# Kernel tuning notes

Hardware: AMD Instinct MI355X
Metric: run time of the kernel (lower is better)

Reference implementation:

```python
import jax, jax.numpy as jnp
import numpy as np
from jax import lax

WINDOW_SIZE = 11
SIGMA = 1.5
C1 = 0.01 ** 2
C2 = 0.03 ** 2


def _gaussian_window(size, sigma):
    coords = np.arange(size, dtype=np.float32) - size // 2
    g = np.exp(-coords ** 2 / (2.0 * sigma ** 2)).astype(np.float32)
    g = g / g.sum()
    w = np.outer(g, g)  # [size, size]
    return jnp.asarray(w)


def _depthwise_conv(x, window2d):
    # x: [B, C, H, W]; window2d: [k, k]
    C = x.shape[1]
    k = window2d.shape[0]
    kernel = jnp.broadcast_to(window2d[None, None], (C, 1, k, k)).astype(x.dtype)
    pad = k // 2
    return lax.conv_general_dilated(
        x, kernel,
        window_strides=(1, 1),
        padding=[(pad, pad), (pad, pad)],
        dimension_numbers=('NCHW', 'OIHW', 'NCHW'),
        feature_group_count=C,
    )


def setup_inputs() -> dict:
    key = jax.random.key(0)
    k1, k2 = jax.random.split(key)
    shape = (32, 3, 512, 512)
    pred = jax.random.uniform(k1, shape, dtype=jnp.float32)
    target = jax.random.uniform(k2, shape, dtype=jnp.float32)
    return {"pred": pred, "target": target}


def reference(pred, target):
    window = _gaussian_window(WINDOW_SIZE, SIGMA)
    mu1 = _depthwise_conv(pred, window)
    mu2 = _depthwise_conv(target, window)
    mu1_sq = mu1 * mu1
    mu2_sq = mu2 * mu2
    mu1_mu2 = mu1 * mu2
    sigma1_sq = _depthwise_conv(pred * pred, window) - mu1_sq
    sigma2_sq = _depthwise_conv(target * target, window) - mu2_sq
    sigma12 = _depthwise_conv(pred * target, window) - mu1_mu2
    ssim_map = ((2.0 * mu1_mu2 + C1) * (2.0 * sigma12 + C2)) / (
        (mu1_sq + mu2_sq + C1) * (sigma1_sq + sigma2_sq + C2))
    return 1.0 - ssim_map.mean()
```

## Files before the change

kernel.cpp:

```cpp
#include <hip/hip_runtime.h>


typedef float f32x2 __attribute__((ext_vector_type(2)));
typedef unsigned int u32;

#define IH 512
#define IW 512
#define TH 4
#define TW 256
#define PW 266
#define RRN 14
#define LPW 268
#define HTILES 128
#define NTILE 24576
#define CPX 3072
#define NPIX 25165824.0f
#define NTHR 320

constexpr float GW[11] = {
    0.00102838f, 0.00759877f, 0.03600078f, 0.10936070f, 0.21300554f,
    0.26601173f,
    0.21300554f, 0.10936070f, 0.03600078f, 0.00759877f, 0.00102838f
};
constexpr float C1f = 0.0001f;
constexpr float C2f = 0.0009f;

__global__ __launch_bounds__(1024) void ssim_reduce(
    const float* __restrict__ ws, float* __restrict__ out)
{
    __shared__ float wsum[16];
    const int tid = threadIdx.x;
    const float4* w4 = reinterpret_cast<const float4*>(ws);
    float s = 0.0f;
    #pragma unroll
    for (int i = 0; i < 6; ++i) {
        const float4 v = w4[tid + i * 1024];
        s += (v.x + v.y) + (v.z + v.w);
    }
    #pragma unroll
    for (int off = 32; off > 0; off >>= 1) s += __shfl_down(s, off, 64);
    if ((tid & 63) == 0) wsum[tid >> 6] = s;
    __syncthreads();
    if (tid == 0) {
        float t = 0.f;
        #pragma unroll
        for (int i = 0; i < 16; ++i) t += wsum[i];
        out[0] = 1.0f - t * (1.0f / NPIX);
    }
}

__global__ __launch_bounds__(NTHR, 2) void ssim_main(
    const float* __restrict__ pred,
    const float* __restrict__ targ,
    float* __restrict__ ws)
{
    __shared__ __align__(16) f32x2 lds01[TH][LPW];
    __shared__ __align__(16) f32x2 lds23[TH][LPW];
    __shared__ float wsum[5];

    const int tid = threadIdx.x;

    const int b  = blockIdx.x;
    const int tl = (b & 7) * CPX + (b >> 3);
    const int ht = tl & (HTILES - 1);
    const int wt = (tl >> 7) & 1;
    const int bc = tl >> 8;

    const int rbase = ht * TH - 5;
    const float* __restrict__ P = pred + (size_t)bc * (IH * IW);
    const float* __restrict__ T = targ + (size_t)bc * (IH * IW);

    if (tid < PW) {
        const int w = wt * TW - 5 + tid;
        const float wm = ((unsigned)w < (unsigned)IW) ? 1.0f : 0.0f;
        const int wc = w < 0 ? 0 : (w > IW - 1 ? IW - 1 : w);

        float rm[RRN];
        u32 voff[RRN];
        #pragma unroll
        for (int rr = 0; rr < RRN; ++rr) {
            const int h = rbase + rr;
            rm[rr] = ((unsigned)h < (unsigned)IH) ? 1.0f : 0.0f;
            const int hc = h < 0 ? 0 : (h > IH - 1 ? IH - 1 : h);
            voff[rr] = (u32)((hc * IW + wc) * 4);
        }

        float pv[RRN], tv[RRN];
        #pragma unroll
        for (int rr = 0; rr < RRN; ++rr)
            asm volatile("global_load_dword %0, %1, %2"
                         : "=v"(pv[rr]) : "v"(voff[rr]), "s"(P));
        #pragma unroll
        for (int rr = 0; rr < RRN; ++rr)
            asm volatile("global_load_dword %0, %1, %2"
                         : "=v"(tv[rr]) : "v"(voff[rr]), "s"(T));
        asm volatile("s_waitcnt vmcnt(0)" ::: "memory");
        __builtin_amdgcn_sched_barrier(0);

        f32x2 a01[TH], a23[TH];
        #pragma unroll
        for (int ro = 0; ro < TH; ++ro) {
            a01[ro].x = 0.f; a01[ro].y = 0.f;
            a23[ro].x = 0.f; a23[ro].y = 0.f;
        }

        #pragma unroll
        for (int rr = 0; rr < RRN; ++rr) {
            f32x2 s01; s01.x = pv[rr]; s01.y = tv[rr];
            const f32x2 rmv = {rm[rr], rm[rr]};
            s01 = s01 * rmv;
            f32x2 s23;
            s23.x = fmaf(s01.x, s01.x, s01.y * s01.y);
            s23.y = s01.x * s01.y;
            #pragma unroll
            for (int ro = 0; ro < TH; ++ro) {
                const int k = rr - ro;
                if (k >= 0 && k < 11) {
                    const f32x2 g = {GW[k], GW[k]};
                    a01[ro] = __builtin_elementwise_fma(g, s01, a01[ro]);
                    a23[ro] = __builtin_elementwise_fma(g, s23, a23[ro]);
                }
            }
        }
        const f32x2 wmv = {wm, wm};
        #pragma unroll
        for (int ro = 0; ro < TH; ++ro) {
            lds01[ro][tid] = a01[ro] * wmv;
            lds23[ro][tid] = a23[ro] * wmv;
        }
    }
    __syncthreads();

    float lsum = 0.0f;
    if (tid < 256) {
        const int r  = tid >> 6;
        const int c0 = (tid & 63) << 2;

        float4 u4[7], v4[7];
        const float4* b01 = reinterpret_cast<const float4*>(&lds01[r][c0]);
        const float4* b23 = reinterpret_cast<const float4*>(&lds23[r][c0]);
        #pragma unroll
        for (int q = 0; q < 7; ++q) { u4[q] = b01[q]; v4[q] = b23[q]; }
        const f32x2* x01 = reinterpret_cast<const f32x2*>(u4);
        const f32x2* x23 = reinterpret_cast<const f32x2*>(v4);

        #pragma unroll
        for (int j = 0; j < 4; ++j) {
            f32x2 acc01; acc01.x = 0.f; acc01.y = 0.f;
            f32x2 acc23; acc23.x = 0.f; acc23.y = 0.f;
            #pragma unroll
            for (int k = 0; k < 11; ++k) {
                const f32x2 g = {GW[k], GW[k]};
                acc01 = __builtin_elementwise_fma(g, x01[j + k], acc01);
                acc23 = __builtin_elementwise_fma(g, x23[j + k], acc23);
            }
            const float m1  = acc01.x;
            const float m2  = acc01.y;
            const float sPP = acc23.x;
            const float e12 = acc23.y;
            const float m1m2 = m1 * m2;
            const float msq  = fmaf(m1, m1, m2 * m2);
            const float num = fmaf(2.0f, m1m2, C1f) * fmaf(2.0f, (e12 - m1m2), C2f);
            const float den = (msq + C1f) * ((sPP - msq) + C2f);
            lsum = fmaf(num, __builtin_amdgcn_rcpf(den), lsum);
        }
    }

    #pragma unroll
    for (int off = 32; off > 0; off >>= 1) lsum += __shfl_down(lsum, off, 64);
    const int lane = tid & 63;
    const int wv   = tid >> 6;
    if (lane == 0) wsum[wv] = lsum;
    __syncthreads();
    if (tid == 0) {
        const float bs = wsum[0] + wsum[1] + wsum[2] + wsum[3] + wsum[4];
        ws[b] = bs;
    }
}

extern "C" void kernel_launch(void* const* d_in, const int* in_sizes, int n_in,
                              void* d_out, int out_size, void* d_ws, size_t ws_size,
                              hipStream_t stream) {
    const float* pred = (const float*)d_in[0];
    const float* targ = (const float*)d_in[1];
    float* out = (float*)d_out;
    float* wsf = (float*)d_ws;

    hipLaunchKernelGGL(ssim_main, dim3(NTILE), dim3(NTHR), 0, stream,
                       pred, targ, wsf);
    hipLaunchKernelGGL(ssim_reduce, dim3(1), dim3(1024), 0, stream, wsf, out);
}
```

Baseline: 89.03 us.

## Stream row slabs per block with sliding register window and prefetch

Each block now walks a vertical slab of 16 row-tiles (64 output rows) instead of a single 4-row tile. It keeps a 14-row register window that shifts by 4 rows per step and prefetches the next 4 rows during compute. This cuts the 14/4 vertical halo re-reads of global memory and the per-tile block launch overhead, so the grid drops from 24576 to 1536 blocks. In exchange there are two barriers per step, fewer blocks for latency hiding, a serial loop dependency, and the row-mask multiply only on border slabs.

```diff
diff --git a/kernel.cpp b/kernel.cpp
--- a/kernel.cpp
+++ b/kernel.cpp
@@ -2,18 +2,17 @@
 
 
 typedef float f32x2 __attribute__((ext_vector_type(2)));
-typedef unsigned int u32;
 
 #define IH 512
 #define IW 512
 #define TH 4
 #define TW 256
 #define PW 266
-#define RRN 14
 #define LPW 268
-#define HTILES 128
-#define NTILE 24576
-#define CPX 3072
+#define KT 16
+#define NSLAB 8
+#define NBLK 1536
+#define CPX 192
 #define NPIX 25165824.0f
 #define NTHR 320
 
@@ -25,28 +24,25 @@
 constexpr float C1f = 0.0001f;
 constexpr float C2f = 0.0009f;
 
-__global__ __launch_bounds__(1024) void ssim_reduce(
+__global__ __launch_bounds__(256) void ssim_reduce(
     const float* __restrict__ ws, float* __restrict__ out)
 {
-    __shared__ float wsum[16];
+    __shared__ float wsum[4];
     const int tid = threadIdx.x;
-    const float4* w4 = reinterpret_cast<const float4*>(ws);
     float s = 0.0f;
     #pragma unroll
-    for (int i = 0; i < 6; ++i) {
-        const float4 v = w4[tid + i * 1024];
-        s += (v.x + v.y) + (v.z + v.w);
-    }
+    for (int i = 0; i < 6; ++i) s += ws[tid + i * 256];
     #pragma unroll
     for (int off = 32; off > 0; off >>= 1) s += __shfl_down(s, off, 64);
     if ((tid & 63) == 0) wsum[tid >> 6] = s;
     __syncthreads();
     if (tid == 0) {
-        float t = 0.f;
-        #pragma unroll
-        for (int i = 0; i < 16; ++i) t += wsum[i];
-        out[0] = 1.0f - t * (1.0f / NPIX);
-    }
+        out[0] = 1.0f - (wsum[0] + wsum[1] + wsum[2] + wsum[3]) * (1.0f / NPIX);
+    }
+}
+
+__device__ __forceinline__ int hclamp(int h) {
+    return h < 0 ? 0 : (h > IH - 1 ? IH - 1 : h);
 }
 
 __global__ __launch_bounds__(NTHR, 2) void ssim_main(
@@ -62,107 +58,125 @@
 
     const int b  = blockIdx.x;
     const int tl = (b & 7) * CPX + (b >> 3);
-    const int ht = tl & (HTILES - 1);
-    const int wt = (tl >> 7) & 1;
-    const int bc = tl >> 8;
-
-    const int rbase = ht * TH - 5;
+    const int slab = tl & (NSLAB - 1);
+    const int wt   = (tl >> 3) & 1;
+    const int bc   = tl >> 4;
+    const int j0   = slab * KT;
+
     const float* __restrict__ P = pred + (size_t)bc * (IH * IW);
     const float* __restrict__ T = targ + (size_t)bc * (IH * IW);
 
-    if (tid < PW) {
-        const int w = wt * TW - 5 + tid;
-        const float wm = ((unsigned)w < (unsigned)IW) ? 1.0f : 0.0f;
-        const int wc = w < 0 ? 0 : (w > IW - 1 ? IW - 1 : w);
-
-        float rm[RRN];
-        u32 voff[RRN];
-        #pragma unroll
-        for (int rr = 0; rr < RRN; ++rr) {
-            const int h = rbase + rr;
-            rm[rr] = ((unsigned)h < (unsigned)IH) ? 1.0f : 0.0f;
-            const int hc = h < 0 ? 0 : (h > IH - 1 ? IH - 1 : h);
-            voff[rr] = (u32)((hc * IW + wc) * 4);
-        }
-
-        float pv[RRN], tv[RRN];
-        #pragma unroll
-        for (int rr = 0; rr < RRN; ++rr)
-            asm volatile("global_load_dword %0, %1, %2"
-                         : "=v"(pv[rr]) : "v"(voff[rr]), "s"(P));
-        #pragma unroll
-        for (int rr = 0; rr < RRN; ++rr)
-            asm volatile("global_load_dword %0, %1, %2"
-                         : "=v"(tv[rr]) : "v"(voff[rr]), "s"(T));
-        asm volatile("s_waitcnt vmcnt(0)" ::: "memory");
+    const int w = wt * TW - 5 + tid;
+    const float wm = ((unsigned)w < (unsigned)IW) ? 1.0f : 0.0f;
+    const int wc = w < 0 ? 0 : (w > IW - 1 ? IW - 1 : w);
+    const bool active = tid < PW;
+    const bool border = (slab == 0) || (slab == NSLAB - 1);
+
+    float pv[14], tv[14];
+    float nlp[4], nlt[4];
+    #pragma unroll
+    for (int rr = 0; rr < 14; ++rr) {
+        const int hc = hclamp(4 * j0 - 5 + rr);
+        pv[rr] = P[(size_t)hc * IW + wc];
+        tv[rr] = T[(size_t)hc * IW + wc];
+    }
+    __builtin_amdgcn_sched_barrier(0);
+
+    float lsum = 0.0f;
+    const f32x2 wmv = {wm, wm};
+
+    for (int jj = 0; jj < KT; ++jj) {
+        const int j = j0 + jj;
+
+        if (jj < KT - 1) {
+            #pragma unroll
+            for (int i = 0; i < 4; ++i) {
+                const int hc = hclamp(4 * j + 9 + i);
+                nlp[i] = P[(size_t)hc * IW + wc];
+                nlt[i] = T[(size_t)hc * IW + wc];
+            }
+        }
         __builtin_amdgcn_sched_barrier(0);
 
-        f32x2 a01[TH], a23[TH];
-        #pragma unroll
-        for (int ro = 0; ro < TH; ++ro) {
-            a01[ro].x = 0.f; a01[ro].y = 0.f;
-            a23[ro].x = 0.f; a23[ro].y = 0.f;
-        }
-
-        #pragma unroll
-        for (int rr = 0; rr < RRN; ++rr) {
-            f32x2 s01; s01.x = pv[rr]; s01.y = tv[rr];
-            const f32x2 rmv = {rm[rr], rm[rr]};
-            s01 = s01 * rmv;
-            f32x2 s23;
-            s23.x = fmaf(s01.x, s01.x, s01.y * s01.y);
-            s23.y = s01.x * s01.y;
+        {
+            f32x2 a01[TH], a23[TH];
             #pragma unroll
             for (int ro = 0; ro < TH; ++ro) {
-                const int k = rr - ro;
-                if (k >= 0 && k < 11) {
+                a01[ro].x = 0.f; a01[ro].y = 0.f;
+                a23[ro].x = 0.f; a23[ro].y = 0.f;
+            }
+            #pragma unroll
+            for (int rr = 0; rr < 14; ++rr) {
+                float p = pv[rr], t = tv[rr];
+                if (border) {
+                    const int row = 4 * j - 5 + rr;
+                    const float rmk = ((unsigned)row < (unsigned)IH) ? 1.0f : 0.0f;
+                    p *= rmk; t *= rmk;
+                }
+                f32x2 s01; s01.x = p; s01.y = t;
+                f32x2 s23;
+                s23.x = fmaf(p, p, t * t);
+                s23.y = p * t;
+                #pragma unroll
+                for (int ro = 0; ro < TH; ++ro) {
+                    const int k = rr - ro;
+                    if (k >= 0 && k < 11) {
+                        const f32x2 g = {GW[k], GW[k]};
+                        a01[ro] = __builtin_elementwise_fma(g, s01, a01[ro]);
+                        a23[ro] = __builtin_elementwise_fma(g, s23, a23[ro]);
+                    }
+                }
+            }
+            if (active) {
+                #pragma unroll
+                for (int ro = 0; ro < TH; ++ro) {
+                    lds01[ro][tid] = a01[ro] * wmv;
+                    lds23[ro][tid] = a23[ro] * wmv;
+                }
+            }
+        }
+        __syncthreads();
+
+        if (tid < 256) {
+            const int r  = tid >> 6;
+            const int c0 = (tid & 63) << 2;
+
+            float4 u4[7], v4[7];
+            const float4* b01 = reinterpret_cast<const float4*>(&lds01[r][c0]);
+            const float4* b23 = reinterpret_cast<const float4*>(&lds23[r][c0]);
+            #pragma unroll
+            for (int q = 0; q < 7; ++q) { u4[q] = b01[q]; v4[q] = b23[q]; }
+            const f32x2* x01 = reinterpret_cast<const f32x2*>(u4);
+            const f32x2* x23 = reinterpret_cast<const f32x2*>(v4);
+
+            #pragma unroll
+            for (int jo = 0; jo < 4; ++jo) {
+                f32x2 acc01; acc01.x = 0.f; acc01.y = 0.f;
+                f32x2 acc23; acc23.x = 0.f; acc23.y = 0.f;
+                #pragma unroll
+                for (int k = 0; k < 11; ++k) {
                     const f32x2 g = {GW[k], GW[k]};
-                    a01[ro] = __builtin_elementwise_fma(g, s01, a01[ro]);
-                    a23[ro] = __builtin_elementwise_fma(g, s23, a23[ro]);
-                }
-            }
-        }
-        const f32x2 wmv = {wm, wm};
-        #pragma unroll
-        for (int ro = 0; ro < TH; ++ro) {
-            lds01[ro][tid] = a01[ro] * wmv;
-            lds23[ro][tid] = a23[ro] * wmv;
-        }
-    }
-    __syncthreads();
-
-    float lsum = 0.0f;
-    if (tid < 256) {
-        const int r  = tid >> 6;
-        const int c0 = (tid & 63) << 2;
-
-        float4 u4[7], v4[7];
-        const float4* b01 = reinterpret_cast<const float4*>(&lds01[r][c0]);
-        const float4* b23 = reinterpret_cast<const float4*>(&lds23[r][c0]);
-        #pragma unroll
-        for (int q = 0; q < 7; ++q) { u4[q] = b01[q]; v4[q] = b23[q]; }
-        const f32x2* x01 = reinterpret_cast<const f32x2*>(u4);
-        const f32x2* x23 = reinterpret_cast<const f32x2*>(v4);
-
-        #pragma unroll
-        for (int j = 0; j < 4; ++j) {
-            f32x2 acc01; acc01.x = 0.f; acc01.y = 0.f;
-            f32x2 acc23; acc23.x = 0.f; acc23.y = 0.f;
-            #pragma unroll
-            for (int k = 0; k < 11; ++k) {
-                const f32x2 g = {GW[k], GW[k]};
-                acc01 = __builtin_elementwise_fma(g, x01[j + k], acc01);
-                acc23 = __builtin_elementwise_fma(g, x23[j + k], acc23);
-            }
-            const float m1  = acc01.x;
-            const float m2  = acc01.y;
-            const float sPP = acc23.x;
-            const float e12 = acc23.y;
-            const float m1m2 = m1 * m2;
-            const float msq  = fmaf(m1, m1, m2 * m2);
-            const float num = fmaf(2.0f, m1m2, C1f) * fmaf(2.0f, (e12 - m1m2), C2f);
-            const float den = (msq + C1f) * ((sPP - msq) + C2f);
-            lsum = fmaf(num, __builtin_amdgcn_rcpf(den), lsum);
+                    acc01 = __builtin_elementwise_fma(g, x01[jo + k], acc01);
+                    acc23 = __builtin_elementwise_fma(g, x23[jo + k], acc23);
+                }
+                const float m1  = acc01.x;
+                const float m2  = acc01.y;
+                const float sPP = acc23.x;
+                const float e12 = acc23.y;
+                const float m1m2 = m1 * m2;
+                const float msq  = fmaf(m1, m1, m2 * m2);
+                const float num = fmaf(2.0f, m1m2, C1f) * fmaf(2.0f, (e12 - m1m2), C2f);
+                const float den = (msq + C1f) * ((sPP - msq) + C2f);
+                lsum = fmaf(num, __builtin_amdgcn_rcpf(den), lsum);
+            }
+        }
+        __syncthreads();
+
+        if (jj < KT - 1) {
+            #pragma unroll
+            for (int i = 0; i < 10; ++i) { pv[i] = pv[i + 4]; tv[i] = tv[i + 4]; }
+            #pragma unroll
+            for (int i = 0; i < 4; ++i)  { pv[10 + i] = nlp[i]; tv[10 + i] = nlt[i]; }
         }
     }
 
@@ -173,8 +187,7 @@
     if (lane == 0) wsum[wv] = lsum;
     __syncthreads();
     if (tid == 0) {
-        const float bs = wsum[0] + wsum[1] + wsum[2] + wsum[3] + wsum[4];
-        ws[b] = bs;
+        ws[b] = wsum[0] + wsum[1] + wsum[2] + wsum[3] + wsum[4];
     }
 }
 
@@ -186,7 +199,7 @@
     float* out = (float*)d_out;
     float* wsf = (float*)d_ws;
 
-    hipLaunchKernelGGL(ssim_main, dim3(NTILE), dim3(NTHR), 0, stream,
+    hipLaunchKernelGGL(ssim_main, dim3(NBLK), dim3(NTHR), 0, stream,
                        pred, targ, wsf);
-    hipLaunchKernelGGL(ssim_reduce, dim3(1), dim3(1024), 0, stream, wsf, out);
-}
+    hipLaunchKernelGGL(ssim_reduce, dim3(1), dim3(256), 0, stream, wsf, out);
+}
```

Result: slower. 129.0 us (+44.8%).

## Cover full image width per block with two columns per thread

Applied to the files above, without the earlier changes.

Each block now processes a full 512-wide row strip instead of a 256-wide half, and each thread loads two adjacent columns as float2. This removes the halo columns that were loaded twice at the split and halves the block count. Width masking is replaced by zero-filled edge pairs, and row masking now runs only on the border tiles. The horizontal pass computes 8 outputs per thread from wider LDS reads. Register use per thread grows, while launch bounds now ask for 4 blocks per CU.

```diff
diff --git a/kernel.cpp b/kernel.cpp
--- a/kernel.cpp
+++ b/kernel.cpp
@@ -2,18 +2,17 @@
 
 
 typedef float f32x2 __attribute__((ext_vector_type(2)));
-typedef unsigned int u32;
 
 #define IH 512
 #define IW 512
 #define TH 4
-#define TW 256
-#define PW 266
-#define RRN 14
-#define LPW 268
+#define NPAIR 262
+#define PSTART 3
+#define PEND 258
+#define LPW 524
 #define HTILES 128
-#define NTILE 24576
-#define CPX 3072
+#define NBLK 12288
+#define CPX 1536
 #define NPIX 25165824.0f
 #define NTHR 320
 
@@ -33,7 +32,7 @@
     const float4* w4 = reinterpret_cast<const float4*>(ws);
     float s = 0.0f;
     #pragma unroll
-    for (int i = 0; i < 6; ++i) {
+    for (int i = 0; i < 3; ++i) {
         const float4 v = w4[tid + i * 1024];
         s += (v.x + v.y) + (v.z + v.w);
     }
@@ -49,7 +48,7 @@
     }
 }
 
-__global__ __launch_bounds__(NTHR, 2) void ssim_main(
+__global__ __launch_bounds__(NTHR, 4) void ssim_main(
     const float* __restrict__ pred,
     const float* __restrict__ targ,
     float* __restrict__ ws)
@@ -63,70 +62,74 @@
     const int b  = blockIdx.x;
     const int tl = (b & 7) * CPX + (b >> 3);
     const int ht = tl & (HTILES - 1);
-    const int wt = (tl >> 7) & 1;
-    const int bc = tl >> 8;
+    const int bc = tl >> 7;
 
     const int rbase = ht * TH - 5;
+    const bool border = (ht == 0) || (ht == HTILES - 1);
     const float* __restrict__ P = pred + (size_t)bc * (IH * IW);
     const float* __restrict__ T = targ + (size_t)bc * (IH * IW);
 
-    if (tid < PW) {
-        const int w = wt * TW - 5 + tid;
-        const float wm = ((unsigned)w < (unsigned)IW) ? 1.0f : 0.0f;
-        const int wc = w < 0 ? 0 : (w > IW - 1 ? IW - 1 : w);
+    if (tid < NPAIR) {
+        const bool hot = (tid >= PSTART) && (tid <= PEND);
+        if (hot) {
+            const int wA = 2 * tid - 6;
+            f32x2 pv[14], tv[14];
+            #pragma unroll
+            for (int rr = 0; rr < 14; ++rr) {
+                const int h = rbase + rr;
+                const int hc = h < 0 ? 0 : (h > IH - 1 ? IH - 1 : h);
+                pv[rr] = *reinterpret_cast<const f32x2*>(P + (size_t)hc * IW + wA);
+                tv[rr] = *reinterpret_cast<const f32x2*>(T + (size_t)hc * IW + wA);
+            }
+            __builtin_amdgcn_sched_barrier(0);
 
-        float rm[RRN];
-        u32 voff[RRN];
-        #pragma unroll
-        for (int rr = 0; rr < RRN; ++rr) {
-            const int h = rbase + rr;
-            rm[rr] = ((unsigned)h < (unsigned)IH) ? 1.0f : 0.0f;
-            const int hc = h < 0 ? 0 : (h > IH - 1 ? IH - 1 : h);
-            voff[rr] = (u32)((hc * IW + wc) * 4);
-        }
-
-        float pv[RRN], tv[RRN];
-        #pragma unroll
-        for (int rr = 0; rr < RRN; ++rr)
-            asm volatile("global_load_dword %0, %1, %2"
-                         : "=v"(pv[rr]) : "v"(voff[rr]), "s"(P));
-        #pragma unroll
-        for (int rr = 0; rr < RRN; ++rr)
-            asm volatile("global_load_dword %0, %1, %2"
-                         : "=v"(tv[rr]) : "v"(voff[rr]), "s"(T));
-        asm volatile("s_waitcnt vmcnt(0)" ::: "memory");
-        __builtin_amdgcn_sched_barrier(0);
-
-        f32x2 a01[TH], a23[TH];
-        #pragma unroll
-        for (int ro = 0; ro < TH; ++ro) {
-            a01[ro].x = 0.f; a01[ro].y = 0.f;
-            a23[ro].x = 0.f; a23[ro].y = 0.f;
-        }
-
-        #pragma unroll
-        for (int rr = 0; rr < RRN; ++rr) {
-            f32x2 s01; s01.x = pv[rr]; s01.y = tv[rr];
-            const f32x2 rmv = {rm[rr], rm[rr]};
-            s01 = s01 * rmv;
-            f32x2 s23;
-            s23.x = fmaf(s01.x, s01.x, s01.y * s01.y);
-            s23.y = s01.x * s01.y;
+            f32x2 aA01[TH], aB01[TH], aA23[TH], aB23[TH];
             #pragma unroll
             for (int ro = 0; ro < TH; ++ro) {
-                const int k = rr - ro;
-                if (k >= 0 && k < 11) {
-                    const f32x2 g = {GW[k], GW[k]};
-                    a01[ro] = __builtin_elementwise_fma(g, s01, a01[ro]);
-                    a23[ro] = __builtin_elementwise_fma(g, s23, a23[ro]);
+                aA01[ro] = (f32x2){0.f, 0.f}; aB01[ro] = (f32x2){0.f, 0.f};
+                aA23[ro] = (f32x2){0.f, 0.f}; aB23[ro] = (f32x2){0.f, 0.f};
+            }
+            #pragma unroll
+            for (int rr = 0; rr < 14; ++rr) {
+                float pA = pv[rr].x, pB = pv[rr].y;
+                float tA = tv[rr].x, tB = tv[rr].y;
+                if (border) {
+                    const float rmk =
+                        ((unsigned)(rbase + rr) < (unsigned)IH) ? 1.0f : 0.0f;
+                    pA *= rmk; pB *= rmk; tA *= rmk; tB *= rmk;
+                }
+                const f32x2 sA01 = {pA, tA};
+                const f32x2 sB01 = {pB, tB};
+                const f32x2 sA23 = {fmaf(pA, pA, tA * tA), pA * tA};
+                const f32x2 sB23 = {fmaf(pB, pB, tB * tB), pB * tB};
+                #pragma unroll
+                for (int ro = 0; ro < TH; ++ro) {
+                    const int k = rr - ro;
+                    if (k >= 0 && k < 11) {
+                        const f32x2 g = {GW[k], GW[k]};
+                        aA01[ro] = __builtin_elementwise_fma(g, sA01, aA01[ro]);
+                        aB01[ro] = __builtin_elementwise_fma(g, sB01, aB01[ro]);
+                        aA23[ro] = __builtin_elementwise_fma(g, sA23, aA23[ro]);
+                        aB23[ro] = __builtin_elementwise_fma(g, sB23, aB23[ro]);
+                    }
                 }
             }
-        }
-        const f32x2 wmv = {wm, wm};
-        #pragma unroll
-        for (int ro = 0; ro < TH; ++ro) {
-            lds01[ro][tid] = a01[ro] * wmv;
-            lds23[ro][tid] = a23[ro] * wmv;
+            #pragma unroll
+            for (int ro = 0; ro < TH; ++ro) {
+                float4 u; u.x = aA01[ro].x; u.y = aA01[ro].y;
+                          u.z = aB01[ro].x; u.w = aB01[ro].y;
+                float4 v; v.x = aA23[ro].x; v.y = aA23[ro].y;
+                          v.z = aB23[ro].x; v.w = aB23[ro].y;
+                *reinterpret_cast<float4*>(&lds01[ro][2 * tid]) = u;
+                *reinterpret_cast<float4*>(&lds23[ro][2 * tid]) = v;
+            }
+        } else {
+            const float4 z = {0.f, 0.f, 0.f, 0.f};
+            #pragma unroll
+            for (int ro = 0; ro < TH; ++ro) {
+                *reinterpret_cast<float4*>(&lds01[ro][2 * tid]) = z;
+                *reinterpret_cast<float4*>(&lds23[ro][2 * tid]) = z;
+            }
         }
     }
     __syncthreads();
@@ -134,25 +137,25 @@
     float lsum = 0.0f;
     if (tid < 256) {
         const int r  = tid >> 6;
-        const int c0 = (tid & 63) << 2;
+        const int c0 = (tid & 63) << 3;
 
-        float4 u4[7], v4[7];
+        float4 u4[10], v4[10];
         const float4* b01 = reinterpret_cast<const float4*>(&lds01[r][c0]);
         const float4* b23 = reinterpret_cast<const float4*>(&lds23[r][c0]);
         #pragma unroll
-        for (int q = 0; q < 7; ++q) { u4[q] = b01[q]; v4[q] = b23[q]; }
+        for (int q = 0; q < 10; ++q) { u4[q] = b01[q]; v4[q] = b23[q]; }
         const f32x2* x01 = reinterpret_cast<const f32x2*>(u4);
         const f32x2* x23 = reinterpret_cast<const f32x2*>(v4);
 
         #pragma unroll
-        for (int j = 0; j < 4; ++j) {
-            f32x2 acc01; acc01.x = 0.f; acc01.y = 0.f;
-            f32x2 acc23; acc23.x = 0.f; acc23.y = 0.f;
+        for (int j = 0; j < 8; ++j) {
+            f32x2 acc01 = {0.f, 0.f};
+            f32x2 acc23 = {0.f, 0.f};
             #pragma unroll
             for (int k = 0; k < 11; ++k) {
                 const f32x2 g = {GW[k], GW[k]};
-                acc01 = __builtin_elementwise_fma(g, x01[j + k], acc01);
-                acc23 = __builtin_elementwise_fma(g, x23[j + k], acc23);
+                acc01 = __builtin_elementwise_fma(g, x01[j + k + 1], acc01);
+                acc23 = __builtin_elementwise_fma(g, x23[j + k + 1], acc23);
             }
             const float m1  = acc01.x;
             const float m2  = acc01.y;
@@ -173,8 +176,7 @@
     if (lane == 0) wsum[wv] = lsum;
     __syncthreads();
     if (tid == 0) {
-        const float bs = wsum[0] + wsum[1] + wsum[2] + wsum[3] + wsum[4];
-        ws[b] = bs;
+        ws[b] = wsum[0] + wsum[1] + wsum[2] + wsum[3] + wsum[4];
     }
 }
 
@@ -186,7 +188,7 @@
     float* out = (float*)d_out;
     float* wsf = (float*)d_ws;
 
-    hipLaunchKernelGGL(ssim_main, dim3(NTILE), dim3(NTHR), 0, stream,
+    hipLaunchKernelGGL(ssim_main, dim3(NBLK), dim3(NTHR), 0, stream,
                        pred, targ, wsf);
     hipLaunchKernelGGL(ssim_reduce, dim3(1), dim3(1024), 0, stream, wsf, out);
 }
```

New measurement: 198.6 us. 2.23x slower.

## Double tile height to 8 rows and fast-path interior tiles without row masks

Applied to the files above, without the earlier changes.

Each block now computes 8 output rows instead of 4, so a 256-wide tile reads 18 input rows instead of 14. This reduces the redundant halo reads and halves the block count, the workspace partials and the final reduction loop. Interior tiles skip the row clamping and mask multiplies and use plain compiler-scheduled loads in place of the inline-asm loads. The trade-off is higher register pressure from 8 accumulator rows and 18 loaded values per thread, which could reduce occupancy, and the loss of the hand-issued load batching.

```diff
diff --git a/kernel.cpp b/kernel.cpp
--- a/kernel.cpp
+++ b/kernel.cpp
@@ -2,18 +2,17 @@
 
 
 typedef float f32x2 __attribute__((ext_vector_type(2)));
-typedef unsigned int u32;
 
 #define IH 512
 #define IW 512
-#define TH 4
+#define TH 8
 #define TW 256
 #define PW 266
-#define RRN 14
+#define RRN 18
 #define LPW 268
-#define HTILES 128
-#define NTILE 24576
-#define CPX 3072
+#define HTILES 64
+#define NBLK 12288
+#define CPX 1536
 #define NPIX 25165824.0f
 #define NTHR 320
 
@@ -33,7 +32,7 @@
     const float4* w4 = reinterpret_cast<const float4*>(ws);
     float s = 0.0f;
     #pragma unroll
-    for (int i = 0; i < 6; ++i) {
+    for (int i = 0; i < 3; ++i) {
         const float4 v = w4[tid + i * 1024];
         s += (v.x + v.y) + (v.z + v.w);
     }
@@ -63,10 +62,11 @@
     const int b  = blockIdx.x;
     const int tl = (b & 7) * CPX + (b >> 3);
     const int ht = tl & (HTILES - 1);
-    const int wt = (tl >> 7) & 1;
-    const int bc = tl >> 8;
+    const int wt = (tl >> 6) & 1;
+    const int bc = tl >> 7;
 
     const int rbase = ht * TH - 5;
+    const bool vint = (ht != 0) && (ht != HTILES - 1);
     const float* __restrict__ P = pred + (size_t)bc * (IH * IW);
     const float* __restrict__ T = targ + (size_t)bc * (IH * IW);
 
@@ -75,43 +75,40 @@
         const float wm = ((unsigned)w < (unsigned)IW) ? 1.0f : 0.0f;
         const int wc = w < 0 ? 0 : (w > IW - 1 ? IW - 1 : w);
 
-        float rm[RRN];
-        u32 voff[RRN];
-        #pragma unroll
-        for (int rr = 0; rr < RRN; ++rr) {
-            const int h = rbase + rr;
-            rm[rr] = ((unsigned)h < (unsigned)IH) ? 1.0f : 0.0f;
-            const int hc = h < 0 ? 0 : (h > IH - 1 ? IH - 1 : h);
-            voff[rr] = (u32)((hc * IW + wc) * 4);
+        float pv[RRN], tv[RRN];
+        if (vint) {
+            const float* __restrict__ Pp = P + (size_t)rbase * IW + wc;
+            const float* __restrict__ Tp = T + (size_t)rbase * IW + wc;
+            #pragma unroll
+            for (int rr = 0; rr < RRN; ++rr) pv[rr] = Pp[(size_t)rr * IW];
+            #pragma unroll
+            for (int rr = 0; rr < RRN; ++rr) tv[rr] = Tp[(size_t)rr * IW];
+        } else {
+            #pragma unroll
+            for (int rr = 0; rr < RRN; ++rr) {
+                const int h = rbase + rr;
+                const int hc = h < 0 ? 0 : (h > IH - 1 ? IH - 1 : h);
+                const float rmk = ((unsigned)h < (unsigned)IH) ? 1.0f : 0.0f;
+                pv[rr] = P[(size_t)hc * IW + wc] * rmk;
+                tv[rr] = T[(size_t)hc * IW + wc] * rmk;
+            }
         }
-
-        float pv[RRN], tv[RRN];
-        #pragma unroll
-        for (int rr = 0; rr < RRN; ++rr)
-            asm volatile("global_load_dword %0, %1, %2"
-                         : "=v"(pv[rr]) : "v"(voff[rr]), "s"(P));
-        #pragma unroll
-        for (int rr = 0; rr < RRN; ++rr)
-            asm volatile("global_load_dword %0, %1, %2"
-                         : "=v"(tv[rr]) : "v"(voff[rr]), "s"(T));
-        asm volatile("s_waitcnt vmcnt(0)" ::: "memory");
         __builtin_amdgcn_sched_barrier(0);
 
         f32x2 a01[TH], a23[TH];
         #pragma unroll
         for (int ro = 0; ro < TH; ++ro) {
-            a01[ro].x = 0.f; a01[ro].y = 0.f;
-            a23[ro].x = 0.f; a23[ro].y = 0.f;
+            a01[ro] = (f32x2){0.f, 0.f};
+            a23[ro] = (f32x2){0.f, 0.f};
         }
 
         #pragma unroll
         for (int rr = 0; rr < RRN; ++rr) {
-            f32x2 s01; s01.x = pv[rr]; s01.y = tv[rr];
-            const f32x2 rmv = {rm[rr], rm[rr]};
-            s01 = s01 * rmv;
+            const float p = pv[rr], t = tv[rr];
+            f32x2 s01; s01.x = p; s01.y = t;
             f32x2 s23;
-            s23.x = fmaf(s01.x, s01.x, s01.y * s01.y);
-            s23.y = s01.x * s01.y;
+            s23.x = fmaf(p, p, t * t);
+            s23.y = p * t;
             #pragma unroll
             for (int ro = 0; ro < TH; ++ro) {
                 const int k = rr - ro;
@@ -133,36 +130,39 @@
 
     float lsum = 0.0f;
     if (tid < 256) {
-        const int r  = tid >> 6;
         const int c0 = (tid & 63) << 2;
+        #pragma unroll
+        for (int half = 0; half < 2; ++half) {
+            const int r = (tid >> 6) + half * 4;
 
-        float4 u4[7], v4[7];
-        const float4* b01 = reinterpret_cast<const float4*>(&lds01[r][c0]);
-        const float4* b23 = reinterpret_cast<const float4*>(&lds23[r][c0]);
-        #pragma unroll
-        for (int q = 0; q < 7; ++q) { u4[q] = b01[q]; v4[q] = b23[q]; }
-        const f32x2* x01 = reinterpret_cast<const f32x2*>(u4);
-        const f32x2* x23 = reinterpret_cast<const f32x2*>(v4);
+            float4 u4[7], v4[7];
+            const float4* b01 = reinterpret_cast<const float4*>(&lds01[r][c0]);
+            const float4* b23 = reinterpret_cast<const float4*>(&lds23[r][c0]);
+            #pragma unroll
+            for (int q = 0; q < 7; ++q) { u4[q] = b01[q]; v4[q] = b23[q]; }
+            const f32x2* x01 = reinterpret_cast<const f32x2*>(u4);
+            const f32x2* x23 = reinterpret_cast<const f32x2*>(v4);
 
-        #pragma unroll
-        for (int j = 0; j < 4; ++j) {
-            f32x2 acc01; acc01.x = 0.f; acc01.y = 0.f;
-            f32x2 acc23; acc23.x = 0.f; acc23.y = 0.f;
             #pragma unroll
-            for (int k = 0; k < 11; ++k) {
-                const f32x2 g = {GW[k], GW[k]};
-                acc01 = __builtin_elementwise_fma(g, x01[j + k], acc01);
-                acc23 = __builtin_elementwise_fma(g, x23[j + k], acc23);
+            for (int j = 0; j < 4; ++j) {
+                f32x2 acc01 = {0.f, 0.f};
+                f32x2 acc23 = {0.f, 0.f};
+                #pragma unroll
+                for (int k = 0; k < 11; ++k) {
+                    const f32x2 g = {GW[k], GW[k]};
+                    acc01 = __builtin_elementwise_fma(g, x01[j + k], acc01);
+                    acc23 = __builtin_elementwise_fma(g, x23[j + k], acc23);
+                }
+                const float m1  = acc01.x;
+                const float m2  = acc01.y;
+                const float sPP = acc23.x;
+                const float e12 = acc23.y;
+                const float m1m2 = m1 * m2;
+                const float msq  = fmaf(m1, m1, m2 * m2);
+                const float num = fmaf(2.0f, m1m2, C1f) * fmaf(2.0f, (e12 - m1m2), C2f);
+                const float den = (msq + C1f) * ((sPP - msq) + C2f);
+                lsum = fmaf(num, __builtin_amdgcn_rcpf(den), lsum);
             }
-            const float m1  = acc01.x;
-            const float m2  = acc01.y;
-            const float sPP = acc23.x;
-            const float e12 = acc23.y;
-            const float m1m2 = m1 * m2;
-            const float msq  = fmaf(m1, m1, m2 * m2);
-            const float num = fmaf(2.0f, m1m2, C1f) * fmaf(2.0f, (e12 - m1m2), C2f);
-            const float den = (msq + C1f) * ((sPP - msq) + C2f);
-            lsum = fmaf(num, __builtin_amdgcn_rcpf(den), lsum);
         }
     }
 
@@ -173,8 +173,7 @@
     if (lane == 0) wsum[wv] = lsum;
     __syncthreads();
     if (tid == 0) {
-        const float bs = wsum[0] + wsum[1] + wsum[2] + wsum[3] + wsum[4];
-        ws[b] = bs;
+        ws[b] = wsum[0] + wsum[1] + wsum[2] + wsum[3] + wsum[4];
     }
 }
 
@@ -186,7 +185,7 @@
     float* out = (float*)d_out;
     float* wsf = (float*)d_ws;
 
-    hipLaunchKernelGGL(ssim_main, dim3(NTILE), dim3(NTHR), 0, stream,
+    hipLaunchKernelGGL(ssim_main, dim3(NBLK), dim3(NTHR), 0, stream,
                        pred, targ, wsf);
     hipLaunchKernelGGL(ssim_reduce, dim3(1), dim3(1024), 0, stream, wsf, out);
 }
```

Result: faster. 85.97 us (-3.4%).
